# Kernel tuning notes

Hardware: AMD Instinct MI355X
Metric: run time of the kernel (lower is better)

The kernel has to match this reference:

```python
import jax, jax.numpy as jnp
import numpy as np

WS = 8          # window size
NUM_HEADS = 8


def setup_inputs() -> dict:
    key = jax.random.key(0)
    k1, k2, k3 = jax.random.split(key, 3)
    B, H, W, C = 8, 192, 192, 256
    x = jax.random.normal(k1, (B, H, W, C), dtype=jnp.float32)
    w_qkv = jax.random.normal(k2, (3 * C, C), dtype=jnp.float32) * (C ** -0.5)
    b_qkv = jnp.zeros((3 * C,), dtype=jnp.float32)
    w_proj = jax.random.normal(k3, (C, C), dtype=jnp.float32) * (C ** -0.5)
    b_proj = jnp.zeros((C,), dtype=jnp.float32)
    return {"x": x, "w_qkv": w_qkv, "b_qkv": b_qkv, "w_proj": w_proj, "b_proj": b_proj}


def _mhsa(tokens, w_qkv, b_qkv, w_proj, b_proj):
    # tokens: [Bgrp, N, C]
    Bg, N, C = tokens.shape
    d = C // NUM_HEADS
    qkv = tokens @ w_qkv.T + b_qkv                      # [Bg, N, 3C]
    qkv = qkv.reshape(Bg, N, 3, NUM_HEADS, d)
    q, k, v = [jnp.transpose(qkv[:, :, i], (0, 2, 1, 3)) for i in range(3)]  # [Bg, h, N, d]
    attn = jax.nn.softmax(jnp.einsum('bhnd,bhmd->bhnm', q, k) * (d ** -0.5), axis=-1)
    out = jnp.einsum('bhnm,bhmd->bhnd', attn, v)        # [Bg, h, N, d]
    out = jnp.transpose(out, (0, 2, 1, 3)).reshape(Bg, N, C)
    return out @ w_proj.T + b_proj


def reference(x, w_qkv, b_qkv, w_proj, b_proj):
    B, H, W, C = x.shape
    nH, nW = H // WS, W // WS
    # window partition: [B, H, W, C] -> [B*nH*nW, WS, WS, C]
    g = x.reshape(B, nH, WS, nW, WS, C).transpose(0, 1, 3, 2, 4, 5)
    tokens = g.reshape(B * nH * nW, WS * WS, C)
    tokens = _mhsa(tokens, w_qkv, b_qkv, w_proj, b_proj)
    # window unpartition
    g = tokens.reshape(B, nH, nW, WS, WS, C).transpose(0, 1, 3, 2, 4, 5)
    return g.reshape(B, H, W, C)
```

## Files before the change

kernel.cpp:

```cpp
#include <hip/hip_runtime.h>

typedef _Float16 half8  __attribute__((ext_vector_type(8)));
typedef _Float16 half4_t __attribute__((ext_vector_type(4)));
typedef __fp16   fp16x2 __attribute__((ext_vector_type(2)));
typedef float    f32x4  __attribute__((ext_vector_type(4)));

union PKU  { fp16x2 h; int i; };
union PK2  { fp16x2 h[2]; int i[2]; half4_t h4; };

__device__ __forceinline__ half4_t mk4(int a, int b) {
  PK2 u; u.i[0] = a; u.i[1] = b; return u.h4;
}

__device__ __forceinline__ int tokIdx(int r, int c) { return r*256 + (c ^ ((r & 7) << 3)); }

__global__ void __launch_bounds__(256)
wconv_kernel(const float* __restrict__ wq, const float* __restrict__ wp,
             _Float16* __restrict__ o)
{
  const int i = (blockIdx.x * 256 + threadIdx.x) * 8;
  const float4 a = *(const float4*)((i < 768*256 ? wq + i : wp + (i - 768*256)));
  const float4 b = *(const float4*)((i < 768*256 ? wq + i + 4 : wp + (i - 768*256) + 4));
  half8 h;
  h[0] = (_Float16)a.x; h[1] = (_Float16)a.y; h[2] = (_Float16)a.z; h[3] = (_Float16)a.w;
  h[4] = (_Float16)b.x; h[5] = (_Float16)b.y; h[6] = (_Float16)b.z; h[7] = (_Float16)b.w;
  *(half8*)(o + i) = h;
}

__global__ void __launch_bounds__(256, 3)
attn_kernel(const float* __restrict__ x,
            const float* __restrict__ b_qkv,
            const float* __restrict__ b_proj,
            const _Float16* __restrict__ w16,
            float* __restrict__ out)
{
  __shared__ __align__(16) _Float16 tok[64*256];

  const int tid  = threadIdx.x;
  const int lane = tid & 63;
  const int w    = tid >> 6;
  const int l15  = lane & 15;
  const int g    = lane >> 4;

  const int wid = blockIdx.x;
  const int b   = wid / (24*24);
  const int wh  = (wid / 24) % 24;
  const int ww  = wid % 24;
  const long long base = (((long long)b*192 + wh*8)*192 + ww*8)*256;

#pragma unroll
  for (int i = 0; i < 16; ++i) {
    const int tk = w*16 + i;
    const f32x4 v = *(const f32x4*)(x + base + ((tk >> 3)*192 + (tk & 7))*256 + lane*4);
    half4_t h;
    h[0] = (_Float16)v[0]; h[1] = (_Float16)v[1];
    h[2] = (_Float16)v[2]; h[3] = (_Float16)v[3];
    *(half4_t*)(tok + tk*256 + ((lane*4) ^ ((tk & 7) << 3))) = h;
  }
  __syncthreads();

  const _Float16* wqkv16  = w16;
  const _Float16* wproj16 = w16 + 768*256;

  const float ALPHA = 0.17677669529663687f;

  int ohp[2][2][4][2];

#pragma unroll
  for (int hi = 0; hi < 2; ++hi) {
    const int hd = 2*w + hi;

    int qtp[2][4][2];
    {
      f32x4 qa[2][4];
#pragma unroll
      for (int mi = 0; mi < 2; ++mi)
#pragma unroll
        for (int ni = 0; ni < 4; ++ni) qa[mi][ni] = (f32x4)0.0f;
#pragma unroll
      for (int kk = 0; kk < 8; ++kk) {
        half8 bt[4], aw[2];
#pragma unroll
        for (int ni = 0; ni < 4; ++ni)
          bt[ni] = *(const half8*)(tok + tokIdx(ni*16 + l15, kk*32 + g*8));
#pragma unroll
        for (int mi = 0; mi < 2; ++mi)
          aw[mi] = *(const half8*)(wqkv16 + (hd*32 + mi*16 + l15)*256 + kk*32 + g*8);
        __builtin_amdgcn_s_setprio(1);
#pragma unroll
        for (int mi = 0; mi < 2; ++mi)
#pragma unroll
          for (int ni = 0; ni < 4; ++ni)
            qa[mi][ni] = __builtin_amdgcn_mfma_f32_16x16x32_f16(aw[mi], bt[ni], qa[mi][ni], 0, 0, 0);
        __builtin_amdgcn_s_setprio(0);
      }
#pragma unroll
      for (int mi = 0; mi < 2; ++mi) {
        float bq[4];
#pragma unroll
        for (int r = 0; r < 4; ++r) bq[r] = b_qkv[hd*32 + mi*16 + g*4 + r];
#pragma unroll
        for (int ni = 0; ni < 4; ++ni) {
          PKU u0, u1;
          u0.h = __builtin_amdgcn_cvt_pkrtz((qa[mi][ni][0] + bq[0])*ALPHA, (qa[mi][ni][1] + bq[1])*ALPHA);
          u1.h = __builtin_amdgcn_cvt_pkrtz((qa[mi][ni][2] + bq[2])*ALPHA, (qa[mi][ni][3] + bq[3])*ALPHA);
          qtp[mi][ni][0] = u0.i; qtp[mi][ni][1] = u1.i;
        }
      }
    }

    int kcp[2][4][2];
    {
      f32x4 kc[2][4];
#pragma unroll
      for (int mi = 0; mi < 2; ++mi)
#pragma unroll
        for (int ni = 0; ni < 4; ++ni) kc[mi][ni] = (f32x4)0.0f;
#pragma unroll
      for (int kk = 0; kk < 8; ++kk) {
        half8 bt[4], aw[2];
#pragma unroll
        for (int ni = 0; ni < 4; ++ni)
          bt[ni] = *(const half8*)(tok + tokIdx(ni*16 + l15, kk*32 + g*8));
#pragma unroll
        for (int mi = 0; mi < 2; ++mi)
          aw[mi] = *(const half8*)(wqkv16 + (256 + hd*32 + mi*16 + l15)*256 + kk*32 + g*8);
        __builtin_amdgcn_s_setprio(1);
#pragma unroll
        for (int mi = 0; mi < 2; ++mi)
#pragma unroll
          for (int ni = 0; ni < 4; ++ni)
            kc[mi][ni] = __builtin_amdgcn_mfma_f32_16x16x32_f16(aw[mi], bt[ni], kc[mi][ni], 0, 0, 0);
        __builtin_amdgcn_s_setprio(0);
      }
#pragma unroll
      for (int mi = 0; mi < 2; ++mi) {
        float bk[4];
#pragma unroll
        for (int r = 0; r < 4; ++r) bk[r] = b_qkv[256 + hd*32 + mi*16 + g*4 + r];
#pragma unroll
        for (int ni = 0; ni < 4; ++ni) {
          PKU u0, u1;
          u0.h = __builtin_amdgcn_cvt_pkrtz(kc[mi][ni][0] + bk[0], kc[mi][ni][1] + bk[1]);
          u1.h = __builtin_amdgcn_cvt_pkrtz(kc[mi][ni][2] + bk[2], kc[mi][ni][3] + bk[3]);
          kcp[mi][ni][0] = u0.i; kcp[mi][ni][1] = u1.i;
        }
      }
    }

    int vpk[4][2][2];
    {
      f32x4 vv[4][2];
#pragma unroll
      for (int mi = 0; mi < 4; ++mi)
#pragma unroll
        for (int ni = 0; ni < 2; ++ni) vv[mi][ni] = (f32x4)0.0f;
#pragma unroll
      for (int kk = 0; kk < 8; ++kk) {
        half8 bt[4], wv[2];
#pragma unroll
        for (int mi = 0; mi < 4; ++mi)
          bt[mi] = *(const half8*)(tok + tokIdx(mi*16 + l15, kk*32 + g*8));
#pragma unroll
        for (int ni = 0; ni < 2; ++ni)
          wv[ni] = *(const half8*)(wqkv16 + (512 + hd*32 + ni*16 + l15)*256 + kk*32 + g*8);
        __builtin_amdgcn_s_setprio(1);
#pragma unroll
        for (int mi = 0; mi < 4; ++mi)
#pragma unroll
          for (int ni = 0; ni < 2; ++ni)
            vv[mi][ni] = __builtin_amdgcn_mfma_f32_16x16x32_f16(bt[mi], wv[ni], vv[mi][ni], 0, 0, 0);
        __builtin_amdgcn_s_setprio(0);
      }
#pragma unroll
      for (int ni = 0; ni < 2; ++ni) {
        const float bv = b_qkv[512 + hd*32 + ni*16 + l15];
#pragma unroll
        for (int mi = 0; mi < 4; ++mi) {
          PKU u0, u1;
          u0.h = __builtin_amdgcn_cvt_pkrtz(vv[mi][ni][0] + bv, vv[mi][ni][1] + bv);
          u1.h = __builtin_amdgcn_cvt_pkrtz(vv[mi][ni][2] + bv, vv[mi][ni][3] + bv);
          vpk[mi][ni][0] = u0.i;
          vpk[mi][ni][1] = u1.i;
        }
      }
    }

    int pk[4][4][2];
    float rv[4];
#pragma unroll
    for (int pr = 0; pr < 2; ++pr) {
      f32x4 s[4][2];
#pragma unroll
      for (int MI = 0; MI < 4; ++MI)
#pragma unroll
        for (int nj = 0; nj < 2; ++nj) s[MI][nj] = (f32x4)0.0f;
      __builtin_amdgcn_s_setprio(1);
#pragma unroll
      for (int kk2 = 0; kk2 < 2; ++kk2)
#pragma unroll
        for (int nj = 0; nj < 2; ++nj) {
          const int ni = pr*2 + nj;
          const half4_t qb = mk4(qtp[kk2][ni][0], qtp[kk2][ni][1]);
#pragma unroll
          for (int MI = 0; MI < 4; ++MI)
            s[MI][nj] = __builtin_amdgcn_mfma_f32_16x16x16f16(
                mk4(kcp[kk2][MI][0], kcp[kk2][MI][1]), qb, s[MI][nj], 0, 0, 0);
        }
      __builtin_amdgcn_s_setprio(0);

#pragma unroll
      for (int nj = 0; nj < 2; ++nj) {
        const int ni = pr*2 + nj;
        float m = s[0][nj][0];
#pragma unroll
        for (int MI = 0; MI < 4; ++MI)
#pragma unroll
          for (int r = 0; r < 4; ++r) m = fmaxf(m, s[MI][nj][r]);
        m = fmaxf(m, __shfl_xor(m, 16, 64));
        m = fmaxf(m, __shfl_xor(m, 32, 64));
        float sum = 0.0f;
#pragma unroll
        for (int MI = 0; MI < 4; ++MI)
#pragma unroll
          for (int r = 0; r < 4; ++r) {
            const float e = __expf(s[MI][nj][r] - m);
            sum += e;
            s[MI][nj][r] = e;
          }
        sum += __shfl_xor(sum, 16, 64);
        sum += __shfl_xor(sum, 32, 64);
        rv[ni] = 1.0f / sum;
#pragma unroll
        for (int MI = 0; MI < 4; ++MI) {
          PKU u0, u1;
          u0.h = __builtin_amdgcn_cvt_pkrtz(s[MI][nj][0], s[MI][nj][1]);
          u1.h = __builtin_amdgcn_cvt_pkrtz(s[MI][nj][2], s[MI][nj][3]);
          pk[MI][ni][0] = u0.i;
          pk[MI][ni][1] = u1.i;
        }
      }
    }

    {
      f32x4 oh[2][4];
#pragma unroll
      for (int MI = 0; MI < 2; ++MI)
#pragma unroll
        for (int ni = 0; ni < 4; ++ni) oh[MI][ni] = (f32x4)0.0f;
      __builtin_amdgcn_s_setprio(1);
#pragma unroll
      for (int kk2 = 0; kk2 < 4; ++kk2)
#pragma unroll
        for (int ni = 0; ni < 4; ++ni) {
          const half4_t pb = mk4(pk[kk2][ni][0], pk[kk2][ni][1]);
#pragma unroll
          for (int MI = 0; MI < 2; ++MI)
            oh[MI][ni] = __builtin_amdgcn_mfma_f32_16x16x16f16(
                mk4(vpk[kk2][MI][0], vpk[kk2][MI][1]), pb, oh[MI][ni], 0, 0, 0);
        }
      __builtin_amdgcn_s_setprio(0);
#pragma unroll
      for (int MI = 0; MI < 2; ++MI)
#pragma unroll
        for (int ni = 0; ni < 4; ++ni) {
          PK2 u;
          u.h[0] = __builtin_amdgcn_cvt_pkrtz(oh[MI][ni][0] * rv[ni], oh[MI][ni][1] * rv[ni]);
          u.h[1] = __builtin_amdgcn_cvt_pkrtz(oh[MI][ni][2] * rv[ni], oh[MI][ni][3] * rv[ni]);
          ohp[hi][MI][ni][0] = u.i[0];
          ohp[hi][MI][ni][1] = u.i[1];
        }
    }
  }

  __syncthreads();

#pragma unroll
  for (int hi = 0; hi < 2; ++hi) {
    const int hd = 2*w + hi;
#pragma unroll
    for (int MI = 0; MI < 2; ++MI)
#pragma unroll
      for (int ni = 0; ni < 4; ++ni) {
        PK2 u;
        u.i[0] = ohp[hi][MI][ni][0];
        u.i[1] = ohp[hi][MI][ni][1];
        *(half4_t*)(tok + tokIdx(ni*16 + l15, hd*32 + MI*16 + g*4)) = u.h4;
      }
  }
  __syncthreads();

  f32x4 pa[4][4];
#pragma unroll
  for (int mi = 0; mi < 4; ++mi)
#pragma unroll
    for (int ni = 0; ni < 4; ++ni) pa[mi][ni] = (f32x4)0.0f;

#pragma unroll
  for (int kk = 0; kk < 8; ++kk) {
    half8 af[4], bf[4];
#pragma unroll
    for (int mi = 0; mi < 4; ++mi)
      af[mi] = *(const half8*)(tok + tokIdx(mi*16 + l15, kk*32 + g*8));
#pragma unroll
    for (int ni = 0; ni < 4; ++ni)
      bf[ni] = *(const half8*)(wproj16 + (w*64 + ni*16 + l15)*256 + kk*32 + g*8);
    __builtin_amdgcn_s_setprio(1);
#pragma unroll
    for (int mi = 0; mi < 4; ++mi)
#pragma unroll
      for (int ni = 0; ni < 4; ++ni)
        pa[mi][ni] = __builtin_amdgcn_mfma_f32_16x16x32_f16(af[mi], bf[ni], pa[mi][ni], 0, 0, 0);
    __builtin_amdgcn_s_setprio(0);
  }

#pragma unroll
  for (int ni = 0; ni < 4; ++ni) {
    const float bb = b_proj[w*64 + ni*16 + l15];
#pragma unroll
    for (int mi = 0; mi < 4; ++mi)
#pragma unroll
      for (int r = 0; r < 4; ++r) pa[mi][ni][r] += bb;
  }

  float* tokF = (float*)tok;
#pragma unroll
  for (int p = 0; p < 2; ++p) {
    __syncthreads();
#pragma unroll
    for (int mh = 0; mh < 2; ++mh) {
      const int mi = 2*p + mh;
#pragma unroll
      for (int ni = 0; ni < 4; ++ni)
#pragma unroll
        for (int r = 0; r < 4; ++r) {
          const int tr = mh*16 + g*4 + r;
          tokF[tr*256 + ((w*64 + ni*16 + l15) ^ ((tr & 7) << 2))] = pa[mi][ni][r];
        }
    }
    __syncthreads();
#pragma unroll
    for (int i = 0; i < 8; ++i) {
      const int tr = w*8 + i;
      const int t  = p*32 + tr;
      const long long rowbase = base + ((long long)(t >> 3)*192 + (t & 7))*256;
      const f32x4 v4 = *(const f32x4*)(tokF + tr*256 + ((lane*4) ^ ((tr & 7) << 2)));
      *(f32x4*)(out + rowbase + lane*4) = v4;
    }
  }
}

extern "C" void kernel_launch(void* const* d_in, const int* in_sizes, int n_in,
                              void* d_out, int out_size, void* d_ws, size_t ws_size,
                              hipStream_t stream) {
  const float* x      = (const float*)d_in[0];
  const float* w_qkv  = (const float*)d_in[1];
  const float* b_qkv  = (const float*)d_in[2];
  const float* w_proj = (const float*)d_in[3];
  const float* b_proj = (const float*)d_in[4];
  float* out = (float*)d_out;
  _Float16* w16 = (_Float16*)d_ws;

  wconv_kernel<<<128, 256, 0, stream>>>(w_qkv, w_proj, w16);
  attn_kernel<<<4608, 256, 0, stream>>>(x, b_qkv, b_proj, w16, out);
}
```

Measured before the change: 340.1 us.

## Fuse Q/K projection loops, defer V projection, fold biases into accumulators

```diff
diff --git a/kernel.cpp b/kernel.cpp
--- a/kernel.cpp
+++ b/kernel.cpp
@@ -70,120 +70,49 @@
   for (int hi = 0; hi < 2; ++hi) {
     const int hd = 2*w + hi;
 
-    int qtp[2][4][2];
+    int qtp[2][4][2], kcp[2][4][2];
     {
-      f32x4 qa[2][4];
-#pragma unroll
-      for (int mi = 0; mi < 2; ++mi)
-#pragma unroll
-        for (int ni = 0; ni < 4; ++ni) qa[mi][ni] = (f32x4)0.0f;
+      f32x4 qa[2][4], kc[2][4];
+#pragma unroll
+      for (int mi = 0; mi < 2; ++mi) {
+        const f32x4 bqv = *(const f32x4*)(b_qkv + hd*32 + mi*16 + g*4);
+        const f32x4 bkv = *(const f32x4*)(b_qkv + 256 + hd*32 + mi*16 + g*4);
+#pragma unroll
+        for (int ni = 0; ni < 4; ++ni) { qa[mi][ni] = bqv; kc[mi][ni] = bkv; }
+      }
 #pragma unroll
       for (int kk = 0; kk < 8; ++kk) {
-        half8 bt[4], aw[2];
+        half8 bt[4], awq[2], awk[2];
 #pragma unroll
         for (int ni = 0; ni < 4; ++ni)
           bt[ni] = *(const half8*)(tok + tokIdx(ni*16 + l15, kk*32 + g*8));
 #pragma unroll
+        for (int mi = 0; mi < 2; ++mi) {
+          awq[mi] = *(const half8*)(wqkv16 + (      hd*32 + mi*16 + l15)*256 + kk*32 + g*8);
+          awk[mi] = *(const half8*)(wqkv16 + (256 + hd*32 + mi*16 + l15)*256 + kk*32 + g*8);
+        }
+        __builtin_amdgcn_s_setprio(1);
+#pragma unroll
         for (int mi = 0; mi < 2; ++mi)
-          aw[mi] = *(const half8*)(wqkv16 + (hd*32 + mi*16 + l15)*256 + kk*32 + g*8);
-        __builtin_amdgcn_s_setprio(1);
-#pragma unroll
-        for (int mi = 0; mi < 2; ++mi)
-#pragma unroll
-          for (int ni = 0; ni < 4; ++ni)
-            qa[mi][ni] = __builtin_amdgcn_mfma_f32_16x16x32_f16(aw[mi], bt[ni], qa[mi][ni], 0, 0, 0);
+#pragma unroll
+          for (int ni = 0; ni < 4; ++ni) {
+            qa[mi][ni] = __builtin_amdgcn_mfma_f32_16x16x32_f16(awq[mi], bt[ni], qa[mi][ni], 0, 0, 0);
+            kc[mi][ni] = __builtin_amdgcn_mfma_f32_16x16x32_f16(awk[mi], bt[ni], kc[mi][ni], 0, 0, 0);
+          }
         __builtin_amdgcn_s_setprio(0);
       }
 #pragma unroll
-      for (int mi = 0; mi < 2; ++mi) {
-        float bq[4];
-#pragma unroll
-        for (int r = 0; r < 4; ++r) bq[r] = b_qkv[hd*32 + mi*16 + g*4 + r];
+      for (int mi = 0; mi < 2; ++mi)
 #pragma unroll
         for (int ni = 0; ni < 4; ++ni) {
-          PKU u0, u1;
-          u0.h = __builtin_amdgcn_cvt_pkrtz((qa[mi][ni][0] + bq[0])*ALPHA, (qa[mi][ni][1] + bq[1])*ALPHA);
-          u1.h = __builtin_amdgcn_cvt_pkrtz((qa[mi][ni][2] + bq[2])*ALPHA, (qa[mi][ni][3] + bq[3])*ALPHA);
-          qtp[mi][ni][0] = u0.i; qtp[mi][ni][1] = u1.i;
-        }
-      }
-    }
-
-    int kcp[2][4][2];
-    {
-      f32x4 kc[2][4];
-#pragma unroll
-      for (int mi = 0; mi < 2; ++mi)
-#pragma unroll
-        for (int ni = 0; ni < 4; ++ni) kc[mi][ni] = (f32x4)0.0f;
-#pragma unroll
-      for (int kk = 0; kk < 8; ++kk) {
-        half8 bt[4], aw[2];
-#pragma unroll
-        for (int ni = 0; ni < 4; ++ni)
-          bt[ni] = *(const half8*)(tok + tokIdx(ni*16 + l15, kk*32 + g*8));
-#pragma unroll
-        for (int mi = 0; mi < 2; ++mi)
-          aw[mi] = *(const half8*)(wqkv16 + (256 + hd*32 + mi*16 + l15)*256 + kk*32 + g*8);
-        __builtin_amdgcn_s_setprio(1);
-#pragma unroll
-        for (int mi = 0; mi < 2; ++mi)
-#pragma unroll
-          for (int ni = 0; ni < 4; ++ni)
-            kc[mi][ni] = __builtin_amdgcn_mfma_f32_16x16x32_f16(aw[mi], bt[ni], kc[mi][ni], 0, 0, 0);
-        __builtin_amdgcn_s_setprio(0);
-      }
-#pragma unroll
-      for (int mi = 0; mi < 2; ++mi) {
-        float bk[4];
-#pragma unroll
-        for (int r = 0; r < 4; ++r) bk[r] = b_qkv[256 + hd*32 + mi*16 + g*4 + r];
-#pragma unroll
-        for (int ni = 0; ni < 4; ++ni) {
-          PKU u0, u1;
-          u0.h = __builtin_amdgcn_cvt_pkrtz(kc[mi][ni][0] + bk[0], kc[mi][ni][1] + bk[1]);
-          u1.h = __builtin_amdgcn_cvt_pkrtz(kc[mi][ni][2] + bk[2], kc[mi][ni][3] + bk[3]);
-          kcp[mi][ni][0] = u0.i; kcp[mi][ni][1] = u1.i;
-        }
-      }
-    }
-
-    int vpk[4][2][2];
-    {
-      f32x4 vv[4][2];
-#pragma unroll
-      for (int mi = 0; mi < 4; ++mi)
-#pragma unroll
-        for (int ni = 0; ni < 2; ++ni) vv[mi][ni] = (f32x4)0.0f;
-#pragma unroll
-      for (int kk = 0; kk < 8; ++kk) {
-        half8 bt[4], wv[2];
-#pragma unroll
-        for (int mi = 0; mi < 4; ++mi)
-          bt[mi] = *(const half8*)(tok + tokIdx(mi*16 + l15, kk*32 + g*8));
-#pragma unroll
-        for (int ni = 0; ni < 2; ++ni)
-          wv[ni] = *(const half8*)(wqkv16 + (512 + hd*32 + ni*16 + l15)*256 + kk*32 + g*8);
-        __builtin_amdgcn_s_setprio(1);
-#pragma unroll
-        for (int mi = 0; mi < 4; ++mi)
-#pragma unroll
-          for (int ni = 0; ni < 2; ++ni)
-            vv[mi][ni] = __builtin_amdgcn_mfma_f32_16x16x32_f16(bt[mi], wv[ni], vv[mi][ni], 0, 0, 0);
-        __builtin_amdgcn_s_setprio(0);
-      }
-#pragma unroll
-      for (int ni = 0; ni < 2; ++ni) {
-        const float bv = b_qkv[512 + hd*32 + ni*16 + l15];
-#pragma unroll
-        for (int mi = 0; mi < 4; ++mi) {
-          PKU u0, u1;
-          u0.h = __builtin_amdgcn_cvt_pkrtz(vv[mi][ni][0] + bv, vv[mi][ni][1] + bv);
-          u1.h = __builtin_amdgcn_cvt_pkrtz(vv[mi][ni][2] + bv, vv[mi][ni][3] + bv);
-          vpk[mi][ni][0] = u0.i;
-          vpk[mi][ni][1] = u1.i;
-        }
-      }
+          PKU q0, q1, k0, k1;
+          q0.h = __builtin_amdgcn_cvt_pkrtz(qa[mi][ni][0]*ALPHA, qa[mi][ni][1]*ALPHA);
+          q1.h = __builtin_amdgcn_cvt_pkrtz(qa[mi][ni][2]*ALPHA, qa[mi][ni][3]*ALPHA);
+          k0.h = __builtin_amdgcn_cvt_pkrtz(kc[mi][ni][0], kc[mi][ni][1]);
+          k1.h = __builtin_amdgcn_cvt_pkrtz(kc[mi][ni][2], kc[mi][ni][3]);
+          qtp[mi][ni][0] = q0.i; qtp[mi][ni][1] = q1.i;
+          kcp[mi][ni][0] = k0.i; kcp[mi][ni][1] = k1.i;
+        }
     }
 
     int pk[4][4][2];
@@ -212,22 +141,21 @@
 #pragma unroll
       for (int nj = 0; nj < 2; ++nj) {
         const int ni = pr*2 + nj;
-        float m = s[0][nj][0];
+        float mm[4];
 #pragma unroll
         for (int MI = 0; MI < 4; ++MI)
-#pragma unroll
-          for (int r = 0; r < 4; ++r) m = fmaxf(m, s[MI][nj][r]);
+          mm[MI] = fmaxf(fmaxf(s[MI][nj][0], s[MI][nj][1]), fmaxf(s[MI][nj][2], s[MI][nj][3]));
+        float m = fmaxf(fmaxf(mm[0], mm[1]), fmaxf(mm[2], mm[3]));
         m = fmaxf(m, __shfl_xor(m, 16, 64));
         m = fmaxf(m, __shfl_xor(m, 32, 64));
-        float sum = 0.0f;
-#pragma unroll
-        for (int MI = 0; MI < 4; ++MI)
-#pragma unroll
-          for (int r = 0; r < 4; ++r) {
-            const float e = __expf(s[MI][nj][r] - m);
-            sum += e;
-            s[MI][nj][r] = e;
-          }
+        float ss[4];
+#pragma unroll
+        for (int MI = 0; MI < 4; ++MI) {
+#pragma unroll
+          for (int r = 0; r < 4; ++r) s[MI][nj][r] = __expf(s[MI][nj][r] - m);
+          ss[MI] = (s[MI][nj][0] + s[MI][nj][1]) + (s[MI][nj][2] + s[MI][nj][3]);
+        }
+        float sum = (ss[0] + ss[1]) + (ss[2] + ss[3]);
         sum += __shfl_xor(sum, 16, 64);
         sum += __shfl_xor(sum, 32, 64);
         rv[ni] = 1.0f / sum;
@@ -242,6 +170,44 @@
       }
     }
 
+    int vpk[4][2][2];
+    {
+      f32x4 vv[4][2];
+#pragma unroll
+      for (int ni = 0; ni < 2; ++ni) {
+        const float bv = b_qkv[512 + hd*32 + ni*16 + l15];
+#pragma unroll
+        for (int mi = 0; mi < 4; ++mi) vv[mi][ni] = (f32x4)bv;
+      }
+#pragma unroll
+      for (int kk = 0; kk < 8; ++kk) {
+        half8 bt[4], wv[2];
+#pragma unroll
+        for (int mi = 0; mi < 4; ++mi)
+          bt[mi] = *(const half8*)(tok + tokIdx(mi*16 + l15, kk*32 + g*8));
+#pragma unroll
+        for (int ni = 0; ni < 2; ++ni)
+          wv[ni] = *(const half8*)(wqkv16 + (512 + hd*32 + ni*16 + l15)*256 + kk*32 + g*8);
+        __builtin_amdgcn_s_setprio(1);
+#pragma unroll
+        for (int mi = 0; mi < 4; ++mi)
+#pragma unroll
+          for (int ni = 0; ni < 2; ++ni)
+            vv[mi][ni] = __builtin_amdgcn_mfma_f32_16x16x32_f16(bt[mi], wv[ni], vv[mi][ni], 0, 0, 0);
+        __builtin_amdgcn_s_setprio(0);
+      }
+#pragma unroll
+      for (int ni = 0; ni < 2; ++ni)
+#pragma unroll
+        for (int mi = 0; mi < 4; ++mi) {
+          PKU u0, u1;
+          u0.h = __builtin_amdgcn_cvt_pkrtz(vv[mi][ni][0], vv[mi][ni][1]);
+          u1.h = __builtin_amdgcn_cvt_pkrtz(vv[mi][ni][2], vv[mi][ni][3]);
+          vpk[mi][ni][0] = u0.i;
+          vpk[mi][ni][1] = u1.i;
+        }
+    }
+
     {
       f32x4 oh[2][4];
 #pragma unroll
@@ -292,9 +258,11 @@
 
   f32x4 pa[4][4];
 #pragma unroll
-  for (int mi = 0; mi < 4; ++mi)
-#pragma unroll
-    for (int ni = 0; ni < 4; ++ni) pa[mi][ni] = (f32x4)0.0f;
+  for (int ni = 0; ni < 4; ++ni) {
+    const float bb = b_proj[w*64 + ni*16 + l15];
+#pragma unroll
+    for (int mi = 0; mi < 4; ++mi) pa[mi][ni] = (f32x4)bb;
+  }
 
 #pragma unroll
   for (int kk = 0; kk < 8; ++kk) {
@@ -312,15 +280,6 @@
       for (int ni = 0; ni < 4; ++ni)
         pa[mi][ni] = __builtin_amdgcn_mfma_f32_16x16x32_f16(af[mi], bf[ni], pa[mi][ni], 0, 0, 0);
     __builtin_amdgcn_s_setprio(0);
-  }
-
-#pragma unroll
-  for (int ni = 0; ni < 4; ++ni) {
-    const float bb = b_proj[w*64 + ni*16 + l15];
-#pragma unroll
-    for (int mi = 0; mi < 4; ++mi)
-#pragma unroll
-      for (int r = 0; r < 4; ++r) pa[mi][ni][r] += bb;
   }
 
   float* tokF = (float*)tok;
```

Result: no change. 337.1 us (-0.9%).
